# Kernel optimization log

Hardware: AMD Instinct MI355X
Metric: run time of the kernel (lower is better)

## Reference

```python
import jax, jax.numpy as jnp
import numpy as np

B, S, D, H = 2, 2048, 1024, 16
DH = D // H

def setup_inputs() -> dict:
    key = jax.random.key(0)
    ks = jax.random.split(key, 12)
    inp = {
        'query': jax.random.normal(ks[0], (B, S, D), jnp.float32),
        'key':   jax.random.normal(ks[1], (B, S, D), jnp.float32),
        'value': jax.random.normal(ks[2], (B, S, D), jnp.float32),
        # causal mask: 1.0 where attention is DISALLOWED (added as mask * -1e9)
        'mask': jnp.triu(jnp.ones((S, S), jnp.float32), k=1)[None, None, :, :],
    }
    sc = 1.0 / np.sqrt(D)
    inp['Wq'] = jax.random.normal(ks[3], (D, D), jnp.float32) * sc
    inp['bq'] = jnp.zeros((D,), jnp.float32)
    inp['Wk'] = jax.random.normal(ks[4], (D, D), jnp.float32) * sc
    inp['bk'] = jnp.zeros((D,), jnp.float32)
    inp['Wv'] = jax.random.normal(ks[5], (D, D), jnp.float32) * sc
    inp['bv'] = jnp.zeros((D,), jnp.float32)
    inp['Wo'] = jax.random.normal(ks[6], (D, D), jnp.float32) * sc
    inp['bo'] = jnp.zeros((D,), jnp.float32)
    return inp

def _split_heads(x):
    # [B,S,D] -> [B,H,S,DH]
    b, s, _ = x.shape
    return x.reshape(b, s, H, DH).transpose(0, 2, 1, 3)

def reference(query, key, value, mask, Wq, bq, Wk, bk, Wv, bv, Wo, bo):
    q = _split_heads(query @ Wq + bq)
    k = _split_heads(key @ Wk + bk)
    v = _split_heads(value @ Wv + bv)
    scale = jnp.sqrt(jnp.asarray(DH, jnp.float32))
    # [B,H,S,S] score tensor (naive, unfused — matches original)
    score = jnp.einsum('bhqd,bhkd->bhqk', q, k) / scale
    score = score + mask * (-1e9)
    attn = jax.nn.softmax(score, axis=-1)
    ctx = jnp.einsum('bhqk,bhkd->bhqd', attn, v)
    ctx = ctx.transpose(0, 2, 1, 3).reshape(query.shape[0], -1, D)
    return ctx @ Wo + bo
```

## Files before the change

### kernel.cpp

```cpp
#include <hip/hip_runtime.h>
#include <hip/hip_bf16.h>
#include <stdint.h>


typedef __bf16 bf16;
typedef __bf16 bf16x2v __attribute__((ext_vector_type(2)));
typedef __bf16 bf16x4v __attribute__((ext_vector_type(4)));
typedef __bf16 bf16x8v __attribute__((ext_vector_type(8)));
typedef float  f32x4v  __attribute__((ext_vector_type(4)));
typedef float  f32x16v __attribute__((ext_vector_type(16)));
typedef unsigned int uint32x2v __attribute__((ext_vector_type(2)));

#define MFMA16(a, b, c) __builtin_amdgcn_mfma_f32_16x16x32_bf16((a), (b), (c), 0, 0, 0)
#define MFMA32(a, b, c) __builtin_amdgcn_mfma_f32_32x32x16_bf16((a), (b), (c), 0, 0, 0)

static constexpr int kS = 2048, kD = 1024, kH = 16, kDH = 64, kB = 2, kM = 4096;

__device__ __forceinline__ void gload16(const void* g, void* lds) {
  __builtin_amdgcn_global_load_lds((const __attribute__((address_space(1))) void*)g,
                                   (__attribute__((address_space(3))) void*)lds, 16, 0, 0);
}

__device__ __forceinline__ float fexp2(float x) {
#if __has_builtin(__builtin_amdgcn_exp2f)
  return __builtin_amdgcn_exp2f(x);
#else
  return exp2f(x);
#endif
}

__global__ void __launch_bounds__(256) cvt_x_kernel(
    const float* __restrict__ q, const float* __restrict__ k, const float* __restrict__ v,
    bf16* __restrict__ xq, bf16* __restrict__ xk, bf16* __restrict__ xv) {
  int i = (blockIdx.x * 256 + threadIdx.x) * 4;
  float4 a = *(const float4*)(q + i);
  float4 b = *(const float4*)(k + i);
  float4 c = *(const float4*)(v + i);
  bf16x4v oa = {(bf16)a.x, (bf16)a.y, (bf16)a.z, (bf16)a.w};
  bf16x4v ob = {(bf16)b.x, (bf16)b.y, (bf16)b.z, (bf16)b.w};
  bf16x4v oc = {(bf16)c.x, (bf16)c.y, (bf16)c.z, (bf16)c.w};
  *(bf16x4v*)(xq + i) = oa;
  *(bf16x4v*)(xk + i) = ob;
  *(bf16x4v*)(xv + i) = oc;
}

__global__ void __launch_bounds__(256) cvt_w_kernel(
    const float* __restrict__ w0, const float* __restrict__ w1,
    const float* __restrict__ w2, const float* __restrict__ w3,
    bf16* __restrict__ o0, bf16* __restrict__ o1, bf16* __restrict__ o2, bf16* __restrict__ o3) {
  const float* w = blockIdx.z == 0 ? w0 : blockIdx.z == 1 ? w1 : blockIdx.z == 2 ? w2 : w3;
  bf16* o       = blockIdx.z == 0 ? o0 : blockIdx.z == 1 ? o1 : blockIdx.z == 2 ? o2 : o3;
  __shared__ float t[32][33];
  int tx = threadIdx.x, ty = threadIdx.y;
  int k0 = blockIdx.x * 32, n0 = blockIdx.y * 32;
#pragma unroll
  for (int j = 0; j < 4; ++j)
    t[ty + j * 8][tx] = w[(size_t)(k0 + ty + j * 8) * kD + n0 + tx];
  __syncthreads();
#pragma unroll
  for (int j = 0; j < 4; ++j)
    o[(size_t)(n0 + ty + j * 8) * kD + k0 + tx] = (bf16)t[tx][ty + j * 8];
}

struct GemmArgs {
  const bf16* A;
  const bf16* Wt;
  const float* bias;
  void* out;
  float scale;
  int omode;
};

__global__ void __launch_bounds__(256) gemm_kernel(GemmArgs ga, GemmArgs gb, GemmArgs gc) {
  GemmArgs g = blockIdx.z == 0 ? ga : blockIdx.z == 1 ? gb : gc;
  __shared__ bf16 smem[8192];
  const int tid = threadIdx.x;
  const int wid = tid >> 6, lane = tid & 63;
  const int g4 = lane >> 4, l16 = lane & 15;
  const int m0 = blockIdx.x * 128, n0 = blockIdx.y * 128;
  const int wr = wid >> 1, wc = wid & 1;

  const int row0 = wid * 16 + (lane >> 2);
  const int row1 = 64 + row0;
  const int sw0 = (lane & 3) ^ ((row0 >> 1) & 3);
  const int sw1 = (lane & 3) ^ ((row1 >> 1) & 3);
  const bf16* gA0 = g.A + (size_t)(m0 + row0) * kD + sw0 * 8;
  const bf16* gA1 = g.A + (size_t)(m0 + row1) * kD + sw1 * 8;
  const bf16* gB0 = g.Wt + (size_t)(n0 + row0) * kD + sw0 * 8;
  const bf16* gB1 = g.Wt + (size_t)(n0 + row1) * kD + sw1 * 8;
  bf16* ldsA0 = &smem[wid * 512];
  bf16* ldsA1 = &smem[(4 + wid) * 512];
  bf16* ldsB0 = &smem[4096 + wid * 512];
  bf16* ldsB1 = &smem[4096 + (4 + wid) * 512];

  const int xorv = (l16 >> 1) & 3;
  f32x4v acc[4][4] = {};

  for (int k0 = 0; k0 < kD; k0 += 32) {
    __syncthreads();
    gload16(gA0 + k0, ldsA0);
    gload16(gA1 + k0, ldsA1);
    gload16(gB0 + k0, ldsB0);
    gload16(gB1 + k0, ldsB1);
    __syncthreads();
    bf16x8v af[4], bfr[4];
#pragma unroll
    for (int i = 0; i < 4; ++i) {
      int rowA = wr * 64 + i * 16 + l16;
      af[i] = *(const bf16x8v*)&smem[rowA * 32 + ((g4 ^ xorv) * 8)];
      int rowB = wc * 64 + i * 16 + l16;
      bfr[i] = *(const bf16x8v*)&smem[4096 + rowB * 32 + ((g4 ^ xorv) * 8)];
    }
#pragma unroll
    for (int i = 0; i < 4; ++i)
#pragma unroll
      for (int j = 0; j < 4; ++j)
        acc[i][j] = MFMA16(af[i], bfr[j], acc[i][j]);
  }

#pragma unroll
  for (int j = 0; j < 4; ++j) {
    int col = n0 + wc * 64 + j * 16 + l16;
    float bj = g.bias[col];
#pragma unroll
    for (int i = 0; i < 4; ++i) {
#pragma unroll
      for (int r = 0; r < 4; ++r) {
        int m = m0 + wr * 64 + i * 16 + g4 * 4 + r;
        float val = (acc[i][j][r] + bj) * g.scale;
        if (g.omode == 0) {
          ((float*)g.out)[(size_t)m * kD + col] = val;
        } else {
          int b = m >> 11, s = m & (kS - 1);
          int h = col >> 6, dh = col & 63;
          size_t addr = (g.omode == 1)
                            ? (((size_t)(b * kH + h) * kS + s) * kDH + dh)
                            : (((size_t)(b * kH + h) * kDH + dh) * kS + s);
          ((bf16*)g.out)[addr] = (bf16)val;
        }
      }
    }
  }
}

__global__ void __launch_bounds__(256) attn_kernel(
    const bf16* __restrict__ Qp, const bf16* __restrict__ Kp,
    const bf16* __restrict__ Vt, bf16* __restrict__ ctx) {
  __shared__ bf16 lds[16384];
  const int tid = threadIdx.x;
  const int wid = tid >> 6, lane = tid & 63;
  const int l32 = lane & 31, hi = lane >> 5;
  const int bh = blockIdx.x;
  const int qt = blockIdx.y;
  const int q0 = qt * 128;
  const int qw = q0 + wid * 32;
  const bf16* Qh = Qp + (size_t)bh * kS * kDH;
  const bf16* Kh = Kp + (size_t)bh * kS * kDH;
  const bf16* Vh = Vt + (size_t)bh * kDH * kS;

  bf16x8v qf[4];
#pragma unroll
  for (int kw = 0; kw < 4; ++kw)
    qf[kw] = *(const bf16x8v*)(Qh + (size_t)(qw + l32) * kDH + kw * 16 + hi * 8);

  f32x16v oacc[2] = {};
  float mreg = -1e30f, lsum = 0.f;
  const int q_lane = qw + l32;

  const int nt = (q0 >> 6) + 2;
  const int ntw = (qw >> 6) + 1;

  const int srow = lane >> 3, schk = lane & 7;
  auto stage = [&](int buf, int k0) {
    bf16* kd = &lds[buf * 8192];
    bf16* vd = kd + 4096;
#pragma unroll
    for (int i = 0; i < 2; ++i) {
      int r = wid * 16 + i * 8 + srow;
      int c = schk ^ (r & 7);
      gload16(Kh + (size_t)(k0 + r) * kDH + c * 8, kd + (wid * 2 + i) * 512);
      gload16(Vh + (size_t)r * kS + k0 + c * 8, vd + (wid * 2 + i) * 512);
    }
  };

  stage(0, 0);
  __syncthreads();
  int cur = 0;
  for (int t = 0; t < nt; ++t) {
    const int k0 = t * 64;
    if (t + 1 < nt) stage(cur ^ 1, k0 + 64);
    if (t < ntw) {
      const bf16* kb = &lds[cur * 8192];
      const bf16* vb = kb + 4096;
      f32x16v st[2] = {};
#pragma unroll
      for (int sub = 0; sub < 2; ++sub) {
        int row = sub * 32 + l32;
        const bf16* krow = kb + row * 64;
        int rx = row & 7;
#pragma unroll
        for (int kw = 0; kw < 4; ++kw) {
          int cw = kw * 2 + hi;
          bf16x8v af = *(const bf16x8v*)(krow + ((cw ^ rx) * 8));
          st[sub] = MFMA32(af, qf[kw], st[sub]);
        }
      }
      if (k0 + 63 > qw) {
#pragma unroll
        for (int sub = 0; sub < 2; ++sub)
#pragma unroll
          for (int r = 0; r < 16; ++r) {
            int kv = k0 + sub * 32 + (r & 3) + 8 * (r >> 2) + 4 * hi;
            if (kv > q_lane) st[sub][r] = -1e30f;
          }
      }
      float rm = st[0][0];
#pragma unroll
      for (int sub = 0; sub < 2; ++sub)
#pragma unroll
        for (int r = 0; r < 16; ++r) rm = fmaxf(rm, st[sub][r]);
      {
        uint32x2v sw = __builtin_amdgcn_permlane32_swap(
            __float_as_uint(rm), __float_as_uint(rm), false, false);
        float partner = __uint_as_float(hi ? sw.x : sw.y);
        rm = fmaxf(rm, partner);
      }
      float mn = fmaxf(mreg, rm);
      float al = fexp2(mreg - mn);
      mreg = mn;
      float rs = 0.f;
#pragma unroll
      for (int sub = 0; sub < 2; ++sub)
#pragma unroll
        for (int r = 0; r < 16; ++r) {
          st[sub][r] = fexp2(st[sub][r] - mn);
          rs += st[sub][r];
        }
      {
        uint32x2v sw = __builtin_amdgcn_permlane32_swap(
            __float_as_uint(rs), __float_as_uint(rs), false, false);
        rs += __uint_as_float(hi ? sw.x : sw.y);
      }
      lsum = lsum * al + rs;
#pragma unroll
      for (int s = 0; s < 2; ++s)
#pragma unroll
        for (int r = 0; r < 16; ++r) oacc[s][r] *= al;

      unsigned int w[16];
#pragma unroll
      for (int sub = 0; sub < 2; ++sub)
#pragma unroll
        for (int i = 0; i < 8; ++i) {
          union { bf16x2v h; unsigned int u; } cv;
          cv.h = bf16x2v{(bf16)st[sub][2 * i], (bf16)st[sub][2 * i + 1]};
          w[sub * 8 + i] = cv.u;
        }
      bf16x8v pb[4];
#pragma unroll
      for (int f = 0; f < 4; ++f) {
        uint32x2v r0 = __builtin_amdgcn_permlane32_swap(w[4 * f], w[4 * f + 2], false, false);
        uint32x2v r1 = __builtin_amdgcn_permlane32_swap(w[4 * f + 1], w[4 * f + 3], false, false);
        union { unsigned int u[4]; bf16x8v h; } fu;
        fu.u[0] = r0.x; fu.u[1] = r1.x; fu.u[2] = r0.y; fu.u[3] = r1.y;
        pb[f] = fu.h;
      }
#pragma unroll
      for (int f = 0; f < 4; ++f) {
        int cw = f * 2 + hi;
#pragma unroll
        for (int s = 0; s < 2; ++s) {
          int row = s * 32 + l32;
          bf16x8v vf = *(const bf16x8v*)(vb + row * 64 + ((cw ^ (row & 7)) * 8));
          oacc[s] = MFMA32(vf, pb[f], oacc[s]);
        }
      }
    }
    __syncthreads();
    cur ^= 1;
  }
  float inv = 1.0f / lsum;
  const int b = bh >> 4, h = bh & 15;
  bf16* crow = ctx + (size_t)(b * kS + qw + l32) * kD + h * 64;
#pragma unroll
  for (int s = 0; s < 2; ++s)
#pragma unroll
    for (int rq = 0; rq < 4; ++rq) {
      union { bf16x4v h; uint32x2v u; } pk;
      pk.h = bf16x4v{(bf16)(oacc[s][rq * 4 + 0] * inv), (bf16)(oacc[s][rq * 4 + 1] * inv),
                     (bf16)(oacc[s][rq * 4 + 2] * inv), (bf16)(oacc[s][rq * 4 + 3] * inv)};
      *(uint32x2v*)(crow + 8 * rq + 4 * hi + 32 * s) = pk.u;
    }
}

extern "C" void kernel_launch(void* const* d_in, const int* in_sizes, int n_in,
                              void* d_out, int out_size, void* d_ws, size_t ws_size,
                              hipStream_t stream) {
  (void)in_sizes; (void)n_in; (void)out_size; (void)ws_size;
  const float* q  = (const float*)d_in[0];
  const float* k  = (const float*)d_in[1];
  const float* v  = (const float*)d_in[2];
  const float* Wq = (const float*)d_in[4];
  const float* bq = (const float*)d_in[5];
  const float* Wk = (const float*)d_in[6];
  const float* bk = (const float*)d_in[7];
  const float* Wv = (const float*)d_in[8];
  const float* bv = (const float*)d_in[9];
  const float* Wo = (const float*)d_in[10];
  const float* bo = (const float*)d_in[11];

  char* p = (char*)d_ws;
  auto carve = [&](size_t bytes) {
    char* r = p;
    p += (bytes + 255) & ~(size_t)255;
    return r;
  };
  const size_t XB = (size_t)kM * kD * sizeof(bf16);
  const size_t WB = (size_t)kD * kD * sizeof(bf16);
  bf16* Xq  = (bf16*)carve(XB);
  bf16* Xk  = (bf16*)carve(XB);
  bf16* Xv  = (bf16*)carve(XB);
  bf16* Wtq = (bf16*)carve(WB);
  bf16* Wtk = (bf16*)carve(WB);
  bf16* Wtv = (bf16*)carve(WB);
  bf16* Wto = (bf16*)carve(WB);
  bf16* Qp  = (bf16*)carve(XB);
  bf16* Kp  = (bf16*)carve(XB);
  bf16* Vt  = (bf16*)carve(XB);
  bf16* Ctx = (bf16*)carve(XB);

  cvt_x_kernel<<<dim3(kM * kD / 1024), 256, 0, stream>>>(q, k, v, Xq, Xk, Xv);
  cvt_w_kernel<<<dim3(32, 32, 4), dim3(32, 8, 1), 0, stream>>>(Wq, Wk, Wv, Wo,
                                                               Wtq, Wtk, Wtv, Wto);
  GemmArgs aq{Xq, Wtq, bq, Qp, 0.125f * 1.44269504f, 1};
  GemmArgs ak{Xk, Wtk, bk, Kp, 1.0f, 1};
  GemmArgs av{Xv, Wtv, bv, Vt, 1.0f, 2};
  gemm_kernel<<<dim3(32, 8, 3), 256, 0, stream>>>(aq, ak, av);
  attn_kernel<<<dim3(32, 16), 256, 0, stream>>>(Qp, Kp, Vt, Ctx);
  GemmArgs ao{Ctx, Wto, bo, d_out, 1.0f, 0};
  gemm_kernel<<<dim3(32, 8, 1), 256, 0, stream>>>(ao, ao, ao);
}
```

Baseline: 243.2 us.

## Double-buffer GEMM LDS loads, shrink N tile, and stage epilogue through LDS

The projection GEMM switches to a 128x64 tile, which doubles the grid, and double-buffers the A/B LDS stages so the next k-slice's global-to-LDS loads overlap the current MFMAs. There is now one barrier per iteration instead of two. The epilogue stages accumulators through per-wave LDS scratch so that head-split, transposed and fp32 outputs are written as vectorised contiguous stores instead of scattered scalar ones. In exchange, the smaller N tile lowers arithmetic intensity, and correctness now depends on the hand-placed waitcnt and barrier ordering.

```diff
diff --git a/kernel.cpp b/kernel.cpp
--- a/kernel.cpp
+++ b/kernel.cpp
@@ -11,10 +11,11 @@
 typedef float  f32x16v __attribute__((ext_vector_type(16)));
 typedef unsigned int uint32x2v __attribute__((ext_vector_type(2)));
 
+#define MFMA32(a, b, c) __builtin_amdgcn_mfma_f32_32x32x16_bf16((a), (b), (c), 0, 0, 0)
 #define MFMA16(a, b, c) __builtin_amdgcn_mfma_f32_16x16x32_bf16((a), (b), (c), 0, 0, 0)
-#define MFMA32(a, b, c) __builtin_amdgcn_mfma_f32_32x32x16_bf16((a), (b), (c), 0, 0, 0)
-
-static constexpr int kS = 2048, kD = 1024, kH = 16, kDH = 64, kB = 2, kM = 4096;
+#define LGKM0() asm volatile("s_waitcnt lgkmcnt(0)" ::: "memory")
+
+static constexpr int kS = 2048, kD = 1024, kH = 16, kDH = 64, kM = 4096;
 
 __device__ __forceinline__ void gload16(const void* g, void* lds) {
   __builtin_amdgcn_global_load_lds((const __attribute__((address_space(1))) void*)g,
@@ -73,72 +74,137 @@
 
 __global__ void __launch_bounds__(256) gemm_kernel(GemmArgs ga, GemmArgs gb, GemmArgs gc) {
   GemmArgs g = blockIdx.z == 0 ? ga : blockIdx.z == 1 ? gb : gc;
-  __shared__ bf16 smem[8192];
-  const int tid = threadIdx.x;
-  const int wid = tid >> 6, lane = tid & 63;
+  constexpr int BN = 64, WN = 32, NJ = 2;
+  constexpr int ASZ = 128 * 32;
+  constexpr int BSZ = BN * 32;
+  __shared__ __align__(16) bf16 smem[2 * ASZ + 2 * BSZ];
+  const int tid = threadIdx.x, wid = tid >> 6, lane = tid & 63;
   const int g4 = lane >> 4, l16 = lane & 15;
-  const int m0 = blockIdx.x * 128, n0 = blockIdx.y * 128;
+  const int m0 = blockIdx.x * 128, n0 = blockIdx.y * BN;
   const int wr = wid >> 1, wc = wid & 1;
-
-  const int row0 = wid * 16 + (lane >> 2);
-  const int row1 = 64 + row0;
-  const int sw0 = (lane & 3) ^ ((row0 >> 1) & 3);
-  const int sw1 = (lane & 3) ^ ((row1 >> 1) & 3);
-  const bf16* gA0 = g.A + (size_t)(m0 + row0) * kD + sw0 * 8;
-  const bf16* gA1 = g.A + (size_t)(m0 + row1) * kD + sw1 * 8;
-  const bf16* gB0 = g.Wt + (size_t)(n0 + row0) * kD + sw0 * 8;
-  const bf16* gB1 = g.Wt + (size_t)(n0 + row1) * kD + sw1 * 8;
-  bf16* ldsA0 = &smem[wid * 512];
-  bf16* ldsA1 = &smem[(4 + wid) * 512];
-  bf16* ldsB0 = &smem[4096 + wid * 512];
-  bf16* ldsB1 = &smem[4096 + (4 + wid) * 512];
+  const bf16* Wt = g.Wt;
+
+  auto stageA = [&](int k0, bf16* As) {
+#pragma unroll
+    for (int i = 0; i < 2; ++i) {
+      int id = i * 256 + tid;
+      int row = id >> 2, c = id & 3;
+      gload16(g.A + (size_t)(m0 + row) * kD + k0 + ((c ^ ((row >> 1) & 3)) * 8),
+              As + (i * 256 + wid * 64) * 8);
+    }
+  };
+  auto stageB = [&](int k0, bf16* Bs) {
+    int row = tid >> 2, c = tid & 3;
+    gload16(Wt + (size_t)(n0 + row) * kD + k0 + ((c ^ ((row >> 1) & 3)) * 8),
+            Bs + (wid * 64) * 8);
+  };
 
   const int xorv = (l16 >> 1) & 3;
-  f32x4v acc[4][4] = {};
-
-  for (int k0 = 0; k0 < kD; k0 += 32) {
-    __syncthreads();
-    gload16(gA0 + k0, ldsA0);
-    gload16(gA1 + k0, ldsA1);
-    gload16(gB0 + k0, ldsB0);
-    gload16(gB1 + k0, ldsB1);
-    __syncthreads();
-    bf16x8v af[4], bfr[4];
+  f32x4v acc[4][NJ] = {};
+
+  stageA(0, smem);
+  stageB(0, smem + 2 * ASZ);
+  __syncthreads();
+
+  constexpr int NT = kD / 32;
+  for (int t = 0; t < NT; ++t) {
+    const int c = t & 1;
+    bf16* Asc = smem + c * ASZ;
+    bf16* Bsc = smem + 2 * ASZ + c * BSZ;
+    if (t + 1 < NT) {
+      stageA((t + 1) * 32, smem + (c ^ 1) * ASZ);
+      stageB((t + 1) * 32, smem + 2 * ASZ + (c ^ 1) * BSZ);
+    }
+    bf16x8v af[4], bfr[NJ];
 #pragma unroll
     for (int i = 0; i < 4; ++i) {
       int rowA = wr * 64 + i * 16 + l16;
-      af[i] = *(const bf16x8v*)&smem[rowA * 32 + ((g4 ^ xorv) * 8)];
-      int rowB = wc * 64 + i * 16 + l16;
-      bfr[i] = *(const bf16x8v*)&smem[4096 + rowB * 32 + ((g4 ^ xorv) * 8)];
+      af[i] = *(const bf16x8v*)(Asc + rowA * 32 + ((g4 ^ xorv) * 8));
+    }
+#pragma unroll
+    for (int j = 0; j < NJ; ++j) {
+      int rowB = wc * WN + j * 16 + l16;
+      bfr[j] = *(const bf16x8v*)(Bsc + rowB * 32 + ((g4 ^ xorv) * 8));
     }
 #pragma unroll
     for (int i = 0; i < 4; ++i)
 #pragma unroll
-      for (int j = 0; j < 4; ++j)
+      for (int j = 0; j < NJ; ++j)
         acc[i][j] = MFMA16(af[i], bfr[j], acc[i][j]);
+    __syncthreads();
   }
 
-#pragma unroll
-  for (int j = 0; j < 4; ++j) {
-    int col = n0 + wc * 64 + j * 16 + l16;
-    float bj = g.bias[col];
+  float* bws = (float*)smem + wid * 1152;
+  const int bb = m0 >> 11;
+  const int h = n0 >> 6;
+
+  if (g.omode == 1) {
+    float bj[NJ];
+#pragma unroll
+    for (int j = 0; j < NJ; ++j) bj[j] = g.bias[n0 + wc * WN + j * 16 + l16];
 #pragma unroll
     for (int i = 0; i < 4; ++i) {
 #pragma unroll
-      for (int r = 0; r < 4; ++r) {
-        int m = m0 + wr * 64 + i * 16 + g4 * 4 + r;
-        float val = (acc[i][j][r] + bj) * g.scale;
-        if (g.omode == 0) {
-          ((float*)g.out)[(size_t)m * kD + col] = val;
-        } else {
-          int b = m >> 11, s = m & (kS - 1);
-          int h = col >> 6, dh = col & 63;
-          size_t addr = (g.omode == 1)
-                            ? (((size_t)(b * kH + h) * kS + s) * kDH + dh)
-                            : (((size_t)(b * kH + h) * kDH + dh) * kS + s);
-          ((bf16*)g.out)[addr] = (bf16)val;
-        }
-      }
+      for (int j = 0; j < NJ; ++j)
+#pragma unroll
+        for (int r = 0; r < 4; ++r)
+          bws[(g4 * 4 + r) * 36 + j * 16 + l16] = (acc[i][j][r] + bj[j]) * g.scale;
+      LGKM0();
+#pragma unroll
+      for (int cc = 0; cc < 2; ++cc) {
+        int id = cc * 64 + lane;
+        int row = id >> 3, ch = id & 7;
+        f32x4v v = *(const f32x4v*)(bws + row * 36 + ch * 4);
+        bf16x4v ov = {(bf16)v.x, (bf16)v.y, (bf16)v.z, (bf16)v.w};
+        int srow = (m0 + wr * 64 + i * 16 + row) & (kS - 1);
+        *(bf16x4v*)((bf16*)g.out +
+                    ((size_t)(bb * kH + h) * kS + srow) * kDH + wc * 32 + ch * 4) = ov;
+      }
+      LGKM0();
+    }
+  } else if (g.omode == 2) {
+#pragma unroll
+    for (int j = 0; j < NJ; ++j) {
+      float bj = g.bias[n0 + wc * WN + j * 16 + l16];
+#pragma unroll
+      for (int i = 0; i < 4; ++i)
+#pragma unroll
+        for (int r = 0; r < 4; ++r)
+          bws[l16 * 72 + i * 16 + g4 * 4 + r] = acc[i][j][r] + bj;
+      LGKM0();
+#pragma unroll
+      for (int cc = 0; cc < 4; ++cc) {
+        int id = cc * 64 + lane;
+        int row = id >> 4, c = id & 15;
+        f32x4v v = *(const f32x4v*)(bws + row * 72 + c * 4);
+        bf16x4v ov = {(bf16)v.x, (bf16)v.y, (bf16)v.z, (bf16)v.w};
+        int dh = wc * 32 + j * 16 + row;
+        int sg = (m0 + wr * 64 + c * 4) & (kS - 1);
+        *(bf16x4v*)((bf16*)g.out + ((size_t)(bb * kH + h) * kDH + dh) * kS + sg) = ov;
+      }
+      LGKM0();
+    }
+  } else {
+    float bj[NJ];
+#pragma unroll
+    for (int j = 0; j < NJ; ++j) bj[j] = g.bias[n0 + wc * WN + j * 16 + l16];
+#pragma unroll
+    for (int i = 0; i < 4; ++i) {
+#pragma unroll
+      for (int j = 0; j < NJ; ++j)
+#pragma unroll
+        for (int r = 0; r < 4; ++r)
+          bws[(g4 * 4 + r) * 36 + j * 16 + l16] = acc[i][j][r] + bj[j];
+      LGKM0();
+#pragma unroll
+      for (int cc = 0; cc < 2; ++cc) {
+        int id = cc * 64 + lane;
+        int row = id >> 3, ch = id & 7;
+        f32x4v v = *(const f32x4v*)(bws + row * 36 + ch * 4);
+        int srow = m0 + wr * 64 + i * 16 + row;
+        *(f32x4v*)((float*)g.out + (size_t)srow * kD + n0 + wc * 32 + ch * 4) = v;
+      }
+      LGKM0();
     }
   }
 }
@@ -335,8 +401,8 @@
   GemmArgs aq{Xq, Wtq, bq, Qp, 0.125f * 1.44269504f, 1};
   GemmArgs ak{Xk, Wtk, bk, Kp, 1.0f, 1};
   GemmArgs av{Xv, Wtv, bv, Vt, 1.0f, 2};
-  gemm_kernel<<<dim3(32, 8, 3), 256, 0, stream>>>(aq, ak, av);
+  gemm_kernel<<<dim3(32, 16, 3), 256, 0, stream>>>(aq, ak, av);
   attn_kernel<<<dim3(32, 16), 256, 0, stream>>>(Qp, Kp, Vt, Ctx);
   GemmArgs ao{Ctx, Wto, bo, d_out, 1.0f, 0};
-  gemm_kernel<<<dim3(32, 8, 1), 256, 0, stream>>>(ao, ao, ao);
-}
+  gemm_kernel<<<dim3(32, 16, 1), 256, 0, stream>>>(ao, ao, ao);
+}
```

Result: no change. 239.7 us (-1.5%).
